# Optimization experiments

Measured on AMD Instinct MI355X. Metric: run time of the kernel, lower is better.

The kernel has to match this reference:

```python
import jax, jax.numpy as jnp
import numpy as np
import math

DIM = 1024
N_HEADS = 16
HEAD_DIM = DIM // N_HEADS
BS, SEQ, NNB = 8, 1024, 50
LN_EPS = 1e-12


def setup_inputs() -> dict:
    key = jax.random.key(0)
    ks = jax.random.split(key, 12)
    std = 0.02
    inp = {
        "x": jax.random.normal(ks[0], (BS, SEQ, DIM), jnp.float32),
        "x_neighbor": jax.random.normal(ks[1], (BS, NNB, DIM), jnp.float32),
        "mask": jnp.ones((BS, SEQ), jnp.int32),
        "neighbor_mask": jnp.ones((BS, NNB), jnp.float32),
        "qw": std * jax.random.normal(ks[2], (DIM, DIM), jnp.float32),
        "qb": jnp.zeros((DIM,), jnp.float32),
        "kw": std * jax.random.normal(ks[3], (DIM, DIM), jnp.float32),
        "kb": jnp.zeros((DIM,), jnp.float32),
        "vw": std * jax.random.normal(ks[4], (DIM, DIM), jnp.float32),
        "vb": jnp.zeros((DIM,), jnp.float32),
        "ow": std * jax.random.normal(ks[5], (DIM, DIM), jnp.float32),
        "ob": jnp.zeros((DIM,), jnp.float32),
        "ln_g": jnp.ones((DIM,), jnp.float32),
        "ln_b": jnp.zeros((DIM,), jnp.float32),
    }
    return inp


def _split_heads(t, bs):
    # [bs, s, dim] -> [bs, h, s, dh]
    return t.reshape(bs, -1, N_HEADS, HEAD_DIM).transpose(0, 2, 1, 3)


def reference(x, x_neighbor, mask, neighbor_mask, qw, qb, kw, kb, vw, vb, ow, ob, ln_g, ln_b):
    bs, seq, dim = x.shape
    # mean-pool neighbors with mask
    nm = neighbor_mask[..., None]                      # [bs, nnb, 1]
    xn = (x_neighbor * nm).sum(axis=1) / nm.sum(axis=1)  # [bs, dim]
    query = jnp.broadcast_to(xn[:, None, :], x.shape)    # [bs, seq, dim]

    q = _split_heads(query @ qw.T + qb, bs) / math.sqrt(HEAD_DIM)
    k = _split_heads(x @ kw.T + kb, bs)
    v = _split_heads(x @ vw.T + vb, bs)

    scores = jnp.einsum("bhqd,bhkd->bhqk", q, k)       # [bs, h, seq, seq]
    key_mask = (mask == 0)[:, None, None, :]            # [bs, 1, 1, seq]
    scores = jnp.where(key_mask, -jnp.inf, scores)
    weights = jax.nn.softmax(scores, axis=-1)           # dropout p=0.0 -> no-op
    context = jnp.einsum("bhqk,bhkd->bhqd", weights, v)
    context = context.transpose(0, 2, 1, 3).reshape(bs, seq, dim)
    out = context @ ow.T + ob

    h = out + x
    mu = h.mean(axis=-1, keepdims=True)
    var = ((h - mu) ** 2).mean(axis=-1, keepdims=True)
    return (h - mu) / jnp.sqrt(var + LN_EPS) * ln_g + ln_b
```

## Files before the change

kernel.cpp:

```cpp
#include <hip/hip_runtime.h>
#include <hip/hip_bf16.h>


#define DIM  1024
#define NH   16
#define HD   64
#define BS   8
#define SEQ  1024
#define NNB  50

#define OF_P     16
#define OF_NUMP  131088
#define OF_DENP  4325392
#define OF_XW    4329488
#define OF_CTX   4460560
#define OF_OUTR  4468752

__global__ void k_prep(const float* __restrict__ xnb, const float* __restrict__ nm,
                       const float* __restrict__ qw, const float* __restrict__ qb,
                       const float* __restrict__ kw, float* __restrict__ p){
  int h = blockIdx.x & 15, b = blockIdx.x >> 4;
  int tid = threadIdx.x, wv = tid >> 6, ln = tid & 63;
  __shared__ float xnl[1024];
  __shared__ float qp[256];
  __shared__ float ql[64];
  {
    int d = tid*4;
    float4 acc = {0,0,0,0}; float wsum = 0.f;
    #pragma unroll 10
    for (int n=0; n<NNB; n++){
      float w = nm[b*NNB + n];
      float4 v = *(const float4*)(xnb + (size_t)(b*NNB + n)*DIM + d);
      acc.x += w*v.x; acc.y += w*v.y; acc.z += w*v.z; acc.w += w*v.w;
      wsum += w;
    }
    float inv = 1.f/wsum;
    acc.x*=inv; acc.y*=inv; acc.z*=inv; acc.w*=inv;
    *(float4*)(xnl + d) = acc;
  }
  __syncthreads();
  {
    const float* qrow = qw + (size_t)(h*HD + ln)*DIM + wv*256;
    const float* xrow = xnl + wv*256;
    float part = 0.f;
    #pragma unroll 16
    for (int i=0; i<64; i++){
      float4 a = *(const float4*)(qrow + i*4);
      float4 c = *(const float4*)(xrow + i*4);
      part += a.x*c.x + a.y*c.y + a.z*c.z + a.w*c.w;
    }
    qp[wv*64 + ln] = part;
  }
  __syncthreads();
  if (wv == 0){
    float qv = qp[ln] + qp[64+ln] + qp[128+ln] + qp[192+ln];
    ql[ln] = (qv + qb[h*HD + ln]) * 0.125f;
  }
  __syncthreads();
  {
    int d = tid*4;
    float4 acc = {0,0,0,0};
    #pragma unroll 8
    for (int j=0; j<HD; j++){
      float qj = ql[j];
      float4 kv = *(const float4*)(kw + (size_t)(h*HD + j)*DIM + d);
      acc.x += qj*kv.x; acc.y += qj*kv.y; acc.z += qj*kv.z; acc.w += qj*kv.w;
    }
    *(float4*)(p + (size_t)(b*NH + h)*DIM + d) = acc;
  }
}

__global__ __launch_bounds__(1024, 4)
void k_swp(const float* __restrict__ x, const float* __restrict__ p,
           const int* __restrict__ mask,
           float* __restrict__ nump, float* __restrict__ denp){
  int b = blockIdx.x, sc = blockIdx.y;
  int s0 = sc * 32;
  int tid = threadIdx.x, wv = tid >> 6, ln = tid & 63;
  __shared__ float wf[32*20];

  int hg = wv & 3, sq = wv >> 2;
  float acc[8][4];
  #pragma unroll
  for (int i=0; i<8; i++){ acc[i][0]=0.f; acc[i][1]=0.f; acc[i][2]=0.f; acc[i][3]=0.f; }

  #pragma unroll 1
  for (int kc=0; kc<4; kc++){
    int d = kc*256 + ln*4;
    const float* pb = p + (size_t)(b*NH + hg*4)*DIM + d;
    float4 pr0 = *(const float4*)(pb);
    float4 pr1 = *(const float4*)(pb +   (size_t)DIM);
    float4 pr2 = *(const float4*)(pb + 2*(size_t)DIM);
    float4 pr3 = *(const float4*)(pb + 3*(size_t)DIM);
    const float* xb = x + (size_t)(b*SEQ + s0 + sq*8)*DIM + d;
    #pragma unroll
    for (int sb=0; sb<8; sb+=4){
      float4 xr[4];
      #pragma unroll
      for (int u=0; u<4; u++)
        xr[u] = *(const float4*)(xb + (size_t)(sb+u)*DIM);
      #pragma unroll
      for (int u=0; u<4; u++){
        acc[sb+u][0] += xr[u].x*pr0.x + xr[u].y*pr0.y + xr[u].z*pr0.z + xr[u].w*pr0.w;
        acc[sb+u][1] += xr[u].x*pr1.x + xr[u].y*pr1.y + xr[u].z*pr1.z + xr[u].w*pr1.w;
        acc[sb+u][2] += xr[u].x*pr2.x + xr[u].y*pr2.y + xr[u].z*pr2.z + xr[u].w*pr2.w;
        acc[sb+u][3] += xr[u].x*pr3.x + xr[u].y*pr3.y + xr[u].z*pr3.z + xr[u].w*pr3.w;
      }
    }
  }
  #pragma unroll
  for (int off=1; off<64; off<<=1){
    #pragma unroll
    for (int si=0; si<8; si++){
      acc[si][0] += __shfl_xor(acc[si][0], off, 64);
      acc[si][1] += __shfl_xor(acc[si][1], off, 64);
      acc[si][2] += __shfl_xor(acc[si][2], off, 64);
      acc[si][3] += __shfl_xor(acc[si][3], off, 64);
    }
  }
  if (ln == 0){
    #pragma unroll
    for (int si=0; si<8; si++){
      float4 v; v.x = acc[si][0]; v.y = acc[si][1]; v.z = acc[si][2]; v.w = acc[si][3];
      *(float4*)(wf + (sq*8 + si)*20 + hg*4) = v;
    }
  }
  __syncthreads();
  if (tid < 512){
    int s = tid >> 4, h = tid & 15;
    float sv = wf[s*20 + h];
    wf[s*20 + h] = mask[b*SEQ + s0 + s] ? __expf(sv) : 0.f;
  }
  __syncthreads();
  if (tid < 16){
    float dsum = 0.f;
    #pragma unroll
    for (int ss=0; ss<32; ss++) dsum += wf[ss*20 + tid];
    denp[(sc*BS + b)*NH + tid] = dsum;
  }
  int hg2 = wv >> 2, dc = wv & 3;
  int d = dc*256 + ln*4;
  const float* xbase = x + (size_t)(b*SEQ + s0)*DIM + d;
  float4 a0={0,0,0,0}, a1={0,0,0,0}, a2={0,0,0,0}, a3={0,0,0,0};
  #pragma unroll 2
  for (int sb=0; sb<32; sb+=4){
    float4 xq[4];
    #pragma unroll
    for (int u=0; u<4; u++)
      xq[u] = *(const float4*)(xbase + (size_t)(sb+u)*DIM);
    #pragma unroll
    for (int u=0; u<4; u++){
      float4 w = *(const float4*)(wf + (sb+u)*20 + hg2*4);
      a0.x += xq[u].x*w.x; a0.y += xq[u].y*w.x; a0.z += xq[u].z*w.x; a0.w += xq[u].w*w.x;
      a1.x += xq[u].x*w.y; a1.y += xq[u].y*w.y; a1.z += xq[u].z*w.y; a1.w += xq[u].w*w.y;
      a2.x += xq[u].x*w.z; a2.y += xq[u].y*w.z; a2.z += xq[u].z*w.z; a2.w += xq[u].w*w.z;
      a3.x += xq[u].x*w.w; a3.y += xq[u].y*w.w; a3.z += xq[u].z*w.w; a3.w += xq[u].w*w.w;
    }
  }
  float* dst = nump + (size_t)sc*(BS*NH*DIM) + (size_t)(b*NH + hg2*4)*DIM + d;
  *(float4*)(dst                 ) = a0;
  *(float4*)(dst +   (size_t)DIM ) = a1;
  *(float4*)(dst + 2*(size_t)DIM ) = a2;
  *(float4*)(dst + 3*(size_t)DIM ) = a3;
}

__global__ void k_xwred(const float* __restrict__ nump, const float* __restrict__ denp,
                        float* __restrict__ xw){
  int id = blockIdx.x*256 + threadIdx.x;
  int bh = id >> 10;
  int b = bh >> 4, h = bh & 15;
  float den = 0.f;
  #pragma unroll
  for (int scn=0; scn<32; scn++) den += denp[(scn*BS + b)*NH + h];
  float num = 0.f;
  #pragma unroll
  for (int scn=0; scn<32; scn++) num += nump[(size_t)scn*(BS*NH*DIM) + id];
  xw[id] = num / den;
}

__global__ void k_ctx(const float* __restrict__ xw, const float* __restrict__ vw,
                      const float* __restrict__ vb, float* __restrict__ ctx){
  int wv = threadIdx.x >> 6, ln = threadIdx.x & 63;
  int jo = blockIdx.x*4 + wv;
  int h  = jo >> 6;
  float acc[BS] = {0,0,0,0,0,0,0,0};
  #pragma unroll
  for (int i=0; i<4; i++){
    int d = ln*4 + 256*i;
    float4 vv = *(const float4*)(vw + (size_t)jo*DIM + d);
    #pragma unroll
    for (int b=0; b<BS; b++){
      float4 xv = *(const float4*)(xw + (size_t)(b*NH + h)*DIM + d);
      acc[b] += vv.x*xv.x + vv.y*xv.y + vv.z*xv.z + vv.w*xv.w;
    }
  }
  #pragma unroll
  for (int off=32; off>=1; off>>=1){
    #pragma unroll
    for (int b=0; b<BS; b++) acc[b] += __shfl_down(acc[b], off, 64);
  }
  if (ln == 0){
    float bias = vb[jo];
    #pragma unroll
    for (int b=0; b<BS; b++) ctx[b*DIM + jo] = acc[b] + bias;
  }
}

__global__ void k_outrow(const float* __restrict__ ctx, const float* __restrict__ ow,
                         const float* __restrict__ ob, float* __restrict__ outr){
  int wv = threadIdx.x >> 6, ln = threadIdx.x & 63;
  int io = blockIdx.x*4 + wv;
  float acc[BS] = {0,0,0,0,0,0,0,0};
  #pragma unroll
  for (int i=0; i<4; i++){
    int d = ln*4 + 256*i;
    float4 wt = *(const float4*)(ow + (size_t)io*DIM + d);
    #pragma unroll
    for (int b=0; b<BS; b++){
      float4 cv = *(const float4*)(ctx + b*DIM + d);
      acc[b] += wt.x*cv.x + wt.y*cv.y + wt.z*cv.z + wt.w*cv.w;
    }
  }
  #pragma unroll
  for (int off=32; off>=1; off>>=1){
    #pragma unroll
    for (int b=0; b<BS; b++) acc[b] += __shfl_down(acc[b], off, 64);
  }
  if (ln == 0){
    float bias = ob[io];
    #pragma unroll
    for (int b=0; b<BS; b++) outr[b*DIM + io] = acc[b] + bias;
  }
}

__global__ void k_ln(const float* __restrict__ x, const float* __restrict__ outr,
                     const float* __restrict__ g, const float* __restrict__ bt,
                     float* __restrict__ out){
  int row = blockIdx.x;
  int b = row >> 10;
  size_t base = (size_t)row * DIM;
  int tid = threadIdx.x;
  float4 xv = ((const float4*)(x + base))[tid];
  float4 ov = ((const float4*)(outr + (size_t)b*DIM))[tid];
  float4 h;
  h.x = xv.x + ov.x; h.y = xv.y + ov.y; h.z = xv.z + ov.z; h.w = xv.w + ov.w;
  float s  = h.x + h.y + h.z + h.w;
  float s2 = h.x*h.x + h.y*h.y + h.z*h.z + h.w*h.w;
  #pragma unroll
  for (int off=32; off>=1; off>>=1){
    s  += __shfl_xor(s,  off, 64);
    s2 += __shfl_xor(s2, off, 64);
  }
  __shared__ float r1[4], r2[4];
  int wv = tid >> 6, ln = tid & 63;
  if (ln == 0){ r1[wv] = s; r2[wv] = s2; }
  __syncthreads();
  s  = r1[0] + r1[1] + r1[2] + r1[3];
  s2 = r2[0] + r2[1] + r2[2] + r2[3];
  float mu   = s  * (1.f/1024.f);
  float var  = s2 * (1.f/1024.f) - mu*mu;
  float rstd = rsqrtf(var + 1e-12f);
  float4 gv = ((const float4*)g)[tid];
  float4 bv = ((const float4*)bt)[tid];
  float4 y;
  y.x = (h.x - mu)*rstd*gv.x + bv.x;
  y.y = (h.y - mu)*rstd*gv.y + bv.y;
  y.z = (h.z - mu)*rstd*gv.z + bv.z;
  y.w = (h.w - mu)*rstd*gv.w + bv.w;
  ((float4*)(out + base))[tid] = y;
}

extern "C" void kernel_launch(void* const* d_in, const int* in_sizes, int n_in,
                              void* d_out, int out_size, void* d_ws, size_t ws_size,
                              hipStream_t stream) {
  const float* x    = (const float*)d_in[0];
  const float* xnb  = (const float*)d_in[1];
  const int*   mask = (const int*  )d_in[2];
  const float* nm   = (const float*)d_in[3];
  const float* qw   = (const float*)d_in[4];
  const float* qb   = (const float*)d_in[5];
  const float* kw   = (const float*)d_in[6];
  const float* vw   = (const float*)d_in[8];
  const float* vb   = (const float*)d_in[9];
  const float* ow   = (const float*)d_in[10];
  const float* ob   = (const float*)d_in[11];
  const float* lng  = (const float*)d_in[12];
  const float* lnb  = (const float*)d_in[13];
  float* out = (float*)d_out;

  float* ws   = (float*)d_ws;
  float* p    = ws + OF_P;
  float* nump = ws + OF_NUMP;
  float* denp = ws + OF_DENP;
  float* xw   = ws + OF_XW;
  float* ctx  = ws + OF_CTX;
  float* outr = ws + OF_OUTR;

  k_prep  <<<128,             256,  0, stream>>>(xnb, nm, qw, qb, kw, p);
  k_swp   <<<dim3(BS,32),     1024, 0, stream>>>(x, p, mask, nump, denp);
  k_xwred <<<512,             256,  0, stream>>>(nump, denp, xw);
  k_ctx   <<<256,             256,  0, stream>>>(xw, vw, vb, ctx);
  k_outrow<<<256,             256,  0, stream>>>(ctx, ow, ob, outr);
  k_ln    <<<BS*SEQ,          256,  0, stream>>>(x, outr, lng, lnb, out);
}
```

Baseline: 173.4 us.

## Replace partial-sum buffers and reduction kernel with atomic accumulation

Instead of writing 32 per-chunk partial numerators and denominators and then reducing them in a separate kernel, each k_swp block now atomically adds its partials into a single xw/den buffer that k_prep zeroes first. The division by the softmax denominator moves into the value-projection kernel. This drops one launch and about 16 MB of partial-buffer traffic. In exchange it issues many float atomics (32-way contention per address), and the summation order becomes nondeterministic.

```diff
diff --git a/kernel.cpp b/kernel.cpp
--- a/kernel.cpp
+++ b/kernel.cpp
@@ -10,17 +10,23 @@
 #define NNB  50
 
 #define OF_P     16
-#define OF_NUMP  131088
-#define OF_DENP  4325392
-#define OF_XW    4329488
-#define OF_CTX   4460560
-#define OF_OUTR  4468752
+#define OF_XW    131088
+#define OF_DEN   262160
+#define OF_CTX   262304
+#define OF_OUTR  270512
 
 __global__ void k_prep(const float* __restrict__ xnb, const float* __restrict__ nm,
                        const float* __restrict__ qw, const float* __restrict__ qb,
-                       const float* __restrict__ kw, float* __restrict__ p){
+                       const float* __restrict__ kw, float* __restrict__ p,
+                       float* __restrict__ xw, float* __restrict__ den){
   int h = blockIdx.x & 15, b = blockIdx.x >> 4;
   int tid = threadIdx.x, wv = tid >> 6, ln = tid & 63;
+  {
+    int gid = blockIdx.x*256 + tid;
+    float4 z = {0.f,0.f,0.f,0.f};
+    *(float4*)(xw + (size_t)gid*4) = z;
+    if (gid < BS*NH) den[gid] = 0.f;
+  }
   __shared__ float xnl[1024];
   __shared__ float qp[256];
   __shared__ float ql[64];
@@ -73,7 +79,7 @@
 __global__ __launch_bounds__(1024, 4)
 void k_swp(const float* __restrict__ x, const float* __restrict__ p,
            const int* __restrict__ mask,
-           float* __restrict__ nump, float* __restrict__ denp){
+           float* __restrict__ xw, float* __restrict__ den){
   int b = blockIdx.x, sc = blockIdx.y;
   int s0 = sc * 32;
   int tid = threadIdx.x, wv = tid >> 6, ln = tid & 63;
@@ -136,7 +142,7 @@
     float dsum = 0.f;
     #pragma unroll
     for (int ss=0; ss<32; ss++) dsum += wf[ss*20 + tid];
-    denp[(sc*BS + b)*NH + tid] = dsum;
+    atomicAdd(&den[b*NH + tid], dsum);
   }
   int hg2 = wv >> 2, dc = wv & 3;
   int d = dc*256 + ln*4;
@@ -157,29 +163,23 @@
       a3.x += xq[u].x*w.w; a3.y += xq[u].y*w.w; a3.z += xq[u].z*w.w; a3.w += xq[u].w*w.w;
     }
   }
-  float* dst = nump + (size_t)sc*(BS*NH*DIM) + (size_t)(b*NH + hg2*4)*DIM + d;
-  *(float4*)(dst                 ) = a0;
-  *(float4*)(dst +   (size_t)DIM ) = a1;
-  *(float4*)(dst + 2*(size_t)DIM ) = a2;
-  *(float4*)(dst + 3*(size_t)DIM ) = a3;
-}
-
-__global__ void k_xwred(const float* __restrict__ nump, const float* __restrict__ denp,
-                        float* __restrict__ xw){
-  int id = blockIdx.x*256 + threadIdx.x;
-  int bh = id >> 10;
-  int b = bh >> 4, h = bh & 15;
-  float den = 0.f;
-  #pragma unroll
-  for (int scn=0; scn<32; scn++) den += denp[(scn*BS + b)*NH + h];
-  float num = 0.f;
-  #pragma unroll
-  for (int scn=0; scn<32; scn++) num += nump[(size_t)scn*(BS*NH*DIM) + id];
-  xw[id] = num / den;
-}
-
-__global__ void k_ctx(const float* __restrict__ xw, const float* __restrict__ vw,
-                      const float* __restrict__ vb, float* __restrict__ ctx){
+  float* dst = xw + (size_t)(b*NH + hg2*4)*DIM + d;
+  atomicAdd(dst + 0, a0.x); atomicAdd(dst + 1, a0.y);
+  atomicAdd(dst + 2, a0.z); atomicAdd(dst + 3, a0.w);
+  dst += DIM;
+  atomicAdd(dst + 0, a1.x); atomicAdd(dst + 1, a1.y);
+  atomicAdd(dst + 2, a1.z); atomicAdd(dst + 3, a1.w);
+  dst += DIM;
+  atomicAdd(dst + 0, a2.x); atomicAdd(dst + 1, a2.y);
+  atomicAdd(dst + 2, a2.z); atomicAdd(dst + 3, a2.w);
+  dst += DIM;
+  atomicAdd(dst + 0, a3.x); atomicAdd(dst + 1, a3.y);
+  atomicAdd(dst + 2, a3.z); atomicAdd(dst + 3, a3.w);
+}
+
+__global__ void k_vctx(const float* __restrict__ xw, const float* __restrict__ den,
+                       const float* __restrict__ vw, const float* __restrict__ vb,
+                       float* __restrict__ ctx){
   int wv = threadIdx.x >> 6, ln = threadIdx.x & 63;
   int jo = blockIdx.x*4 + wv;
   int h  = jo >> 6;
@@ -202,7 +202,8 @@
   if (ln == 0){
     float bias = vb[jo];
     #pragma unroll
-    for (int b=0; b<BS; b++) ctx[b*DIM + jo] = acc[b] + bias;
+    for (int b=0; b<BS; b++)
+      ctx[b*DIM + jo] = acc[b] / den[b*NH + h] + bias;
   }
 }
 
@@ -290,16 +291,14 @@
 
   float* ws   = (float*)d_ws;
   float* p    = ws + OF_P;
-  float* nump = ws + OF_NUMP;
-  float* denp = ws + OF_DENP;
   float* xw   = ws + OF_XW;
+  float* den  = ws + OF_DEN;
   float* ctx  = ws + OF_CTX;
   float* outr = ws + OF_OUTR;
 
-  k_prep  <<<128,             256,  0, stream>>>(xnb, nm, qw, qb, kw, p);
-  k_swp   <<<dim3(BS,32),     1024, 0, stream>>>(x, p, mask, nump, denp);
-  k_xwred <<<512,             256,  0, stream>>>(nump, denp, xw);
-  k_ctx   <<<256,             256,  0, stream>>>(xw, vw, vb, ctx);
+  k_prep  <<<128,             256,  0, stream>>>(xnb, nm, qw, qb, kw, p, xw, den);
+  k_swp   <<<dim3(BS,32),     1024, 0, stream>>>(x, p, mask, xw, den);
+  k_vctx  <<<256,             256,  0, stream>>>(xw, den, vw, vb, ctx);
   k_outrow<<<256,             256,  0, stream>>>(ctx, ow, ob, outr);
   k_ln    <<<BS*SEQ,          256,  0, stream>>>(x, outr, lng, lnb, out);
 }
```

After: 240.7 us. +38.8%, slower.

## Replace partial-numerator buffer with exp weights and a separate pooling kernel

Applied to the files above, without the earlier changes.

The score kernel now stores only masked exp weights per position and head instead of per-chunk weighted sums of x. A new pooling kernel loads each batch's weights into LDS, re-reads x, reduces across waves in shared memory and normalises by the summed denominators. This removes the large partial-numerator write and the separate reduction kernel. In exchange, x is read a second time and the pooling grid is only 32 blocks, which may leave most compute units idle.

```diff
diff --git a/kernel.cpp b/kernel.cpp
--- a/kernel.cpp
+++ b/kernel.cpp
@@ -10,11 +10,11 @@
 #define NNB  50
 
 #define OF_P     16
-#define OF_NUMP  131088
-#define OF_DENP  4325392
-#define OF_XW    4329488
-#define OF_CTX   4460560
-#define OF_OUTR  4468752
+#define OF_E     131088
+#define OF_DENP  262160
+#define OF_XW    266256
+#define OF_CTX   397328
+#define OF_OUTR  405520
 
 __global__ void k_prep(const float* __restrict__ xnb, const float* __restrict__ nm,
                        const float* __restrict__ qw, const float* __restrict__ qb,
@@ -73,7 +73,7 @@
 __global__ __launch_bounds__(1024, 4)
 void k_swp(const float* __restrict__ x, const float* __restrict__ p,
            const int* __restrict__ mask,
-           float* __restrict__ nump, float* __restrict__ denp){
+           float* __restrict__ e, float* __restrict__ denp){
   int b = blockIdx.x, sc = blockIdx.y;
   int s0 = sc * 32;
   int tid = threadIdx.x, wv = tid >> 6, ln = tid & 63;
@@ -129,7 +129,9 @@
   if (tid < 512){
     int s = tid >> 4, h = tid & 15;
     float sv = wf[s*20 + h];
-    wf[s*20 + h] = mask[b*SEQ + s0 + s] ? __expf(sv) : 0.f;
+    float ev = mask[b*SEQ + s0 + s] ? __expf(sv) : 0.f;
+    wf[s*20 + h] = ev;
+    e[(size_t)(b*SEQ + s0)*NH + tid] = ev;
   }
   __syncthreads();
   if (tid < 16){
@@ -138,44 +140,68 @@
     for (int ss=0; ss<32; ss++) dsum += wf[ss*20 + tid];
     denp[(sc*BS + b)*NH + tid] = dsum;
   }
-  int hg2 = wv >> 2, dc = wv & 3;
+}
+
+__global__ __launch_bounds__(1024, 4)
+void k_pool(const float* __restrict__ x, const float* __restrict__ e,
+            const float* __restrict__ denp, float* __restrict__ xw){
+  int b = blockIdx.x, dc = blockIdx.y;
+  int tid = threadIdx.x, wv = tid >> 6, ln = tid & 63;
+  int hg = wv & 3, sq = wv >> 2;
+  __shared__ float elds[SEQ*NH];
+  __shared__ float invd[NH];
+  const float* eb = e + (size_t)b*SEQ*NH;
+  #pragma unroll
+  for (int it=0; it<4; it++){
+    int idx = it*4096 + tid*4;
+    *(float4*)(elds + idx) = *(const float4*)(eb + idx);
+  }
+  if (tid < NH){
+    float dsum = 0.f;
+    #pragma unroll
+    for (int sc=0; sc<32; sc++) dsum += denp[(sc*BS + b)*NH + tid];
+    invd[tid] = 1.f/dsum;
+  }
+  __syncthreads();
   int d = dc*256 + ln*4;
-  const float* xbase = x + (size_t)(b*SEQ + s0)*DIM + d;
+  const float* xb = x + (size_t)(b*SEQ + sq*256)*DIM + d;
   float4 a0={0,0,0,0}, a1={0,0,0,0}, a2={0,0,0,0}, a3={0,0,0,0};
-  #pragma unroll 2
-  for (int sb=0; sb<32; sb+=4){
-    float4 xq[4];
-    #pragma unroll
-    for (int u=0; u<4; u++)
-      xq[u] = *(const float4*)(xbase + (size_t)(sb+u)*DIM);
-    #pragma unroll
-    for (int u=0; u<4; u++){
-      float4 w = *(const float4*)(wf + (sb+u)*20 + hg2*4);
+  #pragma unroll 1
+  for (int ss=0; ss<256; ss+=8){
+    float4 xq[8];
+    #pragma unroll
+    for (int u=0; u<8; u++)
+      xq[u] = *(const float4*)(xb + (size_t)(ss+u)*DIM);
+    #pragma unroll
+    for (int u=0; u<8; u++){
+      float4 w = *(const float4*)(elds + (sq*256 + ss + u)*NH + hg*4);
       a0.x += xq[u].x*w.x; a0.y += xq[u].y*w.x; a0.z += xq[u].z*w.x; a0.w += xq[u].w*w.x;
       a1.x += xq[u].x*w.y; a1.y += xq[u].y*w.y; a1.z += xq[u].z*w.y; a1.w += xq[u].w*w.y;
       a2.x += xq[u].x*w.z; a2.y += xq[u].y*w.z; a2.z += xq[u].z*w.z; a2.w += xq[u].w*w.z;
       a3.x += xq[u].x*w.w; a3.y += xq[u].y*w.w; a3.z += xq[u].z*w.w; a3.w += xq[u].w*w.w;
     }
   }
-  float* dst = nump + (size_t)sc*(BS*NH*DIM) + (size_t)(b*NH + hg2*4)*DIM + d;
-  *(float4*)(dst                 ) = a0;
-  *(float4*)(dst +   (size_t)DIM ) = a1;
-  *(float4*)(dst + 2*(size_t)DIM ) = a2;
-  *(float4*)(dst + 3*(size_t)DIM ) = a3;
-}
-
-__global__ void k_xwred(const float* __restrict__ nump, const float* __restrict__ denp,
-                        float* __restrict__ xw){
-  int id = blockIdx.x*256 + threadIdx.x;
-  int bh = id >> 10;
-  int b = bh >> 4, h = bh & 15;
-  float den = 0.f;
-  #pragma unroll
-  for (int scn=0; scn<32; scn++) den += denp[(scn*BS + b)*NH + h];
-  float num = 0.f;
-  #pragma unroll
-  for (int scn=0; scn<32; scn++) num += nump[(size_t)scn*(BS*NH*DIM) + id];
-  xw[id] = num / den;
+  __syncthreads();
+  float4* red = (float4*)elds;
+  red[0*1024 + wv*64 + ln] = a0;
+  red[1*1024 + wv*64 + ln] = a1;
+  red[2*1024 + wv*64 + ln] = a2;
+  red[3*1024 + wv*64 + ln] = a3;
+  __syncthreads();
+  if (sq == 0){
+    #pragma unroll
+    for (int q=0; q<4; q++){
+      float4 s = red[q*1024 + (0*4+hg)*64 + ln];
+      #pragma unroll
+      for (int s4=1; s4<4; s4++){
+        float4 t = red[q*1024 + (s4*4+hg)*64 + ln];
+        s.x += t.x; s.y += t.y; s.z += t.z; s.w += t.w;
+      }
+      float iv = invd[hg*4 + q];
+      s.x *= iv; s.y *= iv; s.z *= iv; s.w *= iv;
+      *(float4*)(xw + (size_t)(b*NH + hg*4 + q)*DIM + d) = s;
+    }
+  }
 }
 
 __global__ void k_ctx(const float* __restrict__ xw, const float* __restrict__ vw,
@@ -290,15 +316,15 @@
 
   float* ws   = (float*)d_ws;
   float* p    = ws + OF_P;
-  float* nump = ws + OF_NUMP;
+  float* e    = ws + OF_E;
   float* denp = ws + OF_DENP;
   float* xw   = ws + OF_XW;
   float* ctx  = ws + OF_CTX;
   float* outr = ws + OF_OUTR;
 
   k_prep  <<<128,             256,  0, stream>>>(xnb, nm, qw, qb, kw, p);
-  k_swp   <<<dim3(BS,32),     1024, 0, stream>>>(x, p, mask, nump, denp);
-  k_xwred <<<512,             256,  0, stream>>>(nump, denp, xw);
+  k_swp   <<<dim3(BS,32),     1024, 0, stream>>>(x, p, mask, e, denp);
+  k_pool  <<<dim3(BS,4),      1024, 0, stream>>>(x, e, denp, xw);
   k_ctx   <<<256,             256,  0, stream>>>(xw, vw, vb, ctx);
   k_outrow<<<256,             256,  0, stream>>>(ctx, ow, ob, outr);
   k_ln    <<<BS*SEQ,          256,  0, stream>>>(x, outr, lng, lnb, out);
```

After: 198.5 us. +14.5%, slower.
